# Kernel optimization log

Measured on AMD Instinct MI355X. Metric: run time of the kernel, lower is better.

## Reference

```python
import jax, jax.numpy as jnp
import numpy as np

N = 100000
E = 1600000
EMBED = 128
HEADS = 8
HEAD_DIM = EMBED // HEADS
EDGE_DIM = 6


def setup_inputs() -> dict:
    key = jax.random.key(0)
    ks = jax.random.split(key, 12)
    s = 0.05
    return {
        "x": jax.random.normal(ks[0], (N, EMBED), jnp.float32),
        "edge_index": jax.random.randint(ks[1], (2, E), 0, N, dtype=jnp.int64),
        "edge_attr": jax.random.normal(ks[2], (E, EDGE_DIM), jnp.float32),
        "Wq": jax.random.normal(ks[3], (EMBED, EMBED), jnp.float32) * s,
        "Wk": jax.random.normal(ks[4], (EMBED, EMBED), jnp.float32) * s,
        "Wv": jax.random.normal(ks[5], (EMBED, EMBED), jnp.float32) * s,
        "We1": jax.random.normal(ks[6], (EDGE_DIM, EMBED), jnp.float32) * s,
        "be1": jnp.zeros((EMBED,), jnp.float32),
        "We2": jax.random.normal(ks[7], (EMBED, HEADS), jnp.float32) * s,
        "be2": jnp.zeros((HEADS,), jnp.float32),
        "Wo": jax.random.normal(ks[8], (EMBED, EMBED), jnp.float32) * s,
        "bo": jnp.zeros((EMBED,), jnp.float32),
    }


def reference(x, edge_index, edge_attr, Wq, Wk, Wv, We1, be1, We2, be2, Wo, bo):
    num_particles = x.shape[0]
    scaling = HEAD_DIM ** (-0.5)
    # node projections -> (N, H, Dh)
    Q = (x @ Wq).reshape(num_particles, HEADS, HEAD_DIM)
    K = (x @ Wk).reshape(num_particles, HEADS, HEAD_DIM)
    V = (x @ Wv).reshape(num_particles, HEADS, HEAD_DIM)
    src, tgt = edge_index[0], edge_index[1]
    # per-edge dot-product scores (E, H)
    attn_scores = jnp.einsum('ehd,ehd->eh', Q[tgt], K[src]) * scaling
    # edge bias: Linear -> exact GELU -> Linear, (E, H)
    edge_bias = jax.nn.gelu(edge_attr @ We1 + be1, approximate=False) @ We2 + be2
    attn_scores = attn_scores + edge_bias
    # segment (scatter) softmax over edges sharing a target node
    seg_max = jax.ops.segment_max(attn_scores, tgt, num_segments=num_particles)
    ex = jnp.exp(attn_scores - seg_max[tgt])
    denom = jax.ops.segment_sum(ex, tgt, num_segments=num_particles)
    attn_weights = ex / denom[tgt]
    # weighted scatter-sum of V_src -> (N, H, Dh)
    weighted_V = attn_weights[:, :, None] * V[src]
    out = jax.ops.segment_sum(weighted_V, tgt, num_segments=num_particles)
    out = out.reshape(num_particles, EMBED) @ Wo + bo
    return out, attn_weights
```

## Files before the change

kernel.cpp:

```cpp
#include <hip/hip_runtime.h>

#define N_NODES 100000
#define N_EDGES 1600000
#define MAXD 64

typedef unsigned int u32;
typedef unsigned short u16;

__device__ __forceinline__ float bf2f(u16 u){ return __uint_as_float(((u32)u) << 16); }
__device__ __forceinline__ float lo16(u32 u){ return __uint_as_float(u << 16); }
__device__ __forceinline__ float hi16(u32 u){ return __uint_as_float(u & 0xffff0000u); }
__device__ __forceinline__ u32 f2bfbits(float f){
  u32 u = __float_as_uint(f);
  return (u + 0x7fffu + ((u >> 16) & 1u)) >> 16;
}

__device__ __forceinline__ float gelu_fast(float h){
  float z = h * 0.70710678118654752f;
  float u = z * z;
  const float k0 = 1.1283791670955126f;
  const float k1 = -0.37612638903183752f;
  const float k2 = 0.11283791670955126f;
  const float k3 = -0.026866170645131251f;
  const float k4 = 0.0052239776254421878f;
  const float k5 = -8.5483270234508528e-4f;
  const float k6 = 1.2055332981789664e-4f;
  float p = __builtin_fmaf(k6, u, k5);
  p = __builtin_fmaf(p, u, k4);
  p = __builtin_fmaf(p, u, k3);
  p = __builtin_fmaf(p, u, k2);
  p = __builtin_fmaf(p, u, k1);
  p = __builtin_fmaf(p, u, k0);
  float er = z * p;
  if (u > 0.36f) er = erff(z);
  float hh = 0.5f * h;
  return __builtin_fmaf(hh, er, hh);
}

template<int DT>
__device__ __forceinline__ float ldf(const void* p, size_t i){
  if (DT) return ((const float*)p)[i];
  else    return bf2f(((const u16*)p)[i]);
}

__device__ __forceinline__ int ld_src(const int* ei, int e, int f64){
  return f64 ? ei[2*(size_t)e] : ei[e];
}
__device__ __forceinline__ int ld_tgt(const int* ei, int e, int f64){
  return f64 ? ei[2*((size_t)N_EDGES + (size_t)e)] : ei[(size_t)N_EDGES + e];
}

__device__ __forceinline__ float bfdot16(uint4 qa, uint4 qb, uint4 ka, uint4 kb){
  float s = 0.f;
  s += lo16(qa.x)*lo16(ka.x) + hi16(qa.x)*hi16(ka.x);
  s += lo16(qa.y)*lo16(ka.y) + hi16(qa.y)*hi16(ka.y);
  s += lo16(qa.z)*lo16(ka.z) + hi16(qa.z)*hi16(ka.z);
  s += lo16(qa.w)*lo16(ka.w) + hi16(qa.w)*hi16(ka.w);
  s += lo16(qb.x)*lo16(kb.x) + hi16(qb.x)*hi16(kb.x);
  s += lo16(qb.y)*lo16(kb.y) + hi16(qb.y)*hi16(kb.y);
  s += lo16(qb.z)*lo16(kb.z) + hi16(qb.z)*hi16(kb.z);
  s += lo16(qb.w)*lo16(kb.w) + hi16(qb.w)*hi16(kb.w);
  return s;
}

extern "C" __global__ void detect_kernel(const int* __restrict__ ei,
                                         const u32* __restrict__ xw,
                                         int* __restrict__ flags)
{
  if (blockIdx.x == 0 && threadIdx.x == 0) {
    int any = 0;
    #pragma unroll
    for (int i = 0; i < 32; ++i) any |= ei[2*i + 1];
    flags[0] = (any == 0) ? 1 : 0;
    int weird = 0;
    for (int i = 0; i < 256; ++i) {
      u32 w = xw[i];
      float a = lo16(w), b = hi16(w);
      if (!(fabsf(a) < 1024.f)) weird++;
      if (!(fabsf(b) < 1024.f)) weird++;
    }
    flags[1] = (weird > 0) ? 1 : 0;
  }
}

template<int DT>
__global__ __launch_bounds__(256) void qkv_gemm_t(
    const void* __restrict__ x, const void* __restrict__ Wq,
    const void* __restrict__ Wk, const void* __restrict__ Wv,
    u16* __restrict__ Q, u16* __restrict__ Kd, u16* __restrict__ Vd,
    const int* __restrict__ flags)
{
  if (flags[1] != DT) return;
  __shared__ float xs[64*129];
  const int tid = threadIdx.x;
  const int row0 = blockIdx.x * 64;
  const void* W = (blockIdx.y == 0) ? Wq : (blockIdx.y == 1) ? Wk : Wv;
  u16* Out = (blockIdx.y == 0) ? Q : (blockIdx.y == 1) ? Kd : Vd;

  if (DT) {
    const float4* xg = (const float4*)x;
    #pragma unroll
    for (int i = 0; i < 8; ++i) {
      int li = tid + i*256;
      int r = li >> 5, c4 = li & 31;
      float4 v = make_float4(0.f,0.f,0.f,0.f);
      if (row0 + r < N_NODES) v = xg[(size_t)(row0 + r)*32 + c4];
      int base = r*129 + c4*4;
      xs[base] = v.x; xs[base+1] = v.y; xs[base+2] = v.z; xs[base+3] = v.w;
    }
  } else {
    const uint4* xg = (const uint4*)x;
    #pragma unroll
    for (int i = 0; i < 4; ++i) {
      int li = tid + i*256;
      int r = li >> 4, c8 = li & 15;
      uint4 v = make_uint4(0,0,0,0);
      if (row0 + r < N_NODES) v = xg[(size_t)(row0 + r)*16 + c8];
      int base = r*129 + c8*8;
      xs[base+0]=lo16(v.x); xs[base+1]=hi16(v.x);
      xs[base+2]=lo16(v.y); xs[base+3]=hi16(v.y);
      xs[base+4]=lo16(v.z); xs[base+5]=hi16(v.z);
      xs[base+6]=lo16(v.w); xs[base+7]=hi16(v.w);
    }
  }
  __syncthreads();

  const int cg = tid & 31;
  const int r0 = (tid >> 5) * 8;
  float acc[8][4];
  #pragma unroll
  for (int i=0;i<8;++i){ acc[i][0]=0.f; acc[i][1]=0.f; acc[i][2]=0.f; acc[i][3]=0.f; }

  for (int k = 0; k < 128; ++k) {
    float4 b;
    if (DT) {
      b = ((const float4*)W)[k*32 + cg];
    } else {
      uint2 t = ((const uint2*)W)[k*32 + cg];
      b = make_float4(lo16(t.x), hi16(t.x), lo16(t.y), hi16(t.y));
    }
    #pragma unroll
    for (int i = 0; i < 8; ++i) {
      float a = xs[(r0+i)*129 + k];
      acc[i][0] += a*b.x; acc[i][1] += a*b.y; acc[i][2] += a*b.z; acc[i][3] += a*b.w;
    }
  }
  #pragma unroll
  for (int i = 0; i < 8; ++i) {
    int gr = row0 + r0 + i;
    if (gr < N_NODES) {
      u32 p0 = f2bfbits(acc[i][0]) | (f2bfbits(acc[i][1]) << 16);
      u32 p1 = f2bfbits(acc[i][2]) | (f2bfbits(acc[i][3]) << 16);
      ((uint2*)(Out + (size_t)gr*128))[cg] = make_uint2(p0, p1);
    }
  }
}

template<int DT>
__global__ __launch_bounds__(256) void bias_kernel_t(
    const void* __restrict__ ea,
    const void* __restrict__ We1, const void* __restrict__ be1,
    const void* __restrict__ We2, const void* __restrict__ be2,
    float* __restrict__ scores, const int* __restrict__ flags)
{
  if (flags[1] != DT) return;
  __shared__ __align__(16) float wpk[128][16];
  __shared__ float b2s[8];
  const int tid = threadIdx.x;
  if (tid < 128) {
    int j = tid;
    wpk[j][0] = ldf<DT>(be1, j);
    #pragma unroll
    for (int d = 0; d < 6; ++d) wpk[j][1+d] = ldf<DT>(We1, d*128 + j);
    wpk[j][7] = 0.f;
    #pragma unroll
    for (int h = 0; h < 8; ++h) wpk[j][8+h] = ldf<DT>(We2, j*8 + h);
  }
  if (tid < 8) b2s[tid] = ldf<DT>(be2, tid);
  __syncthreads();

  const int gid = blockIdx.x * 256 + tid;
  if (gid >= N_EDGES/2) return;
  const int e0 = gid * 2;

  float a[12];
  if (DT) {
    const float4* eg = (const float4*)ea + (size_t)gid*3;
    float4 v0 = eg[0], v1 = eg[1], v2 = eg[2];
    a[0]=v0.x; a[1]=v0.y; a[2]=v0.z; a[3]=v0.w;
    a[4]=v1.x; a[5]=v1.y; a[6]=v1.z; a[7]=v1.w;
    a[8]=v2.x; a[9]=v2.y; a[10]=v2.z; a[11]=v2.w;
  } else {
    const uint2* eg = (const uint2*)ea + (size_t)gid*3;
    uint2 v0 = eg[0], v1 = eg[1], v2 = eg[2];
    u32 d[6] = {v0.x, v0.y, v1.x, v1.y, v2.x, v2.y};
    #pragma unroll
    for (int idx = 0; idx < 12; ++idx)
      a[idx] = (idx & 1) ? hi16(d[idx >> 1]) : lo16(d[idx >> 1]);
  }

  float bias[2][8];
  #pragma unroll
  for (int t=0;t<2;++t)
    #pragma unroll
    for (int h=0;h<8;++h) bias[t][h] = b2s[h];

  for (int j = 0; j < 128; ++j) {
    const float4* wp = (const float4*)wpk[j];
    float4 p0 = wp[0], p1 = wp[1], p2 = wp[2], p3 = wp[3];
    #pragma unroll
    for (int t = 0; t < 2; ++t) {
      float h = p0.x + a[t*6+0]*p0.y + a[t*6+1]*p0.z + a[t*6+2]*p0.w
                     + a[t*6+3]*p1.x + a[t*6+4]*p1.y + a[t*6+5]*p1.z;
      float g = gelu_fast(h);
      bias[t][0] += g*p2.x; bias[t][1] += g*p2.y; bias[t][2] += g*p2.z; bias[t][3] += g*p2.w;
      bias[t][4] += g*p3.x; bias[t][5] += g*p3.y; bias[t][6] += g*p3.z; bias[t][7] += g*p3.w;
    }
  }

  #pragma unroll
  for (int t = 0; t < 2; ++t) {
    float4* so = (float4*)(scores + (size_t)(e0 + t)*8);
    so[0] = make_float4(bias[t][0],bias[t][1],bias[t][2],bias[t][3]);
    so[1] = make_float4(bias[t][4],bias[t][5],bias[t][6],bias[t][7]);
  }
}

extern "C" __global__ __launch_bounds__(256) void hist_kernel(
    const int* __restrict__ ei, int* __restrict__ offs, const int* __restrict__ flags)
{
  int e = blockIdx.x*256 + threadIdx.x;
  if (e >= N_EDGES) return;
  int t = ld_tgt(ei, e, flags[0]);
  atomicAdd(&offs[t], 1);
}

extern "C" __global__ __launch_bounds__(1024) void scan1_kernel(
    int* __restrict__ offs, int* __restrict__ bsums)
{
  __shared__ int tmp[1024];
  int tid = threadIdx.x;
  int i = blockIdx.x*1024 + tid;
  int v = (i < N_NODES) ? offs[i] : 0;
  tmp[tid] = v;
  __syncthreads();
  for (int d = 1; d < 1024; d <<= 1) {
    int t = (tid >= d) ? tmp[tid-d] : 0;
    __syncthreads();
    tmp[tid] += t;
    __syncthreads();
  }
  if (i < N_NODES) offs[i] = tmp[tid] - v;
  if (tid == 1023) bsums[blockIdx.x] = tmp[1023];
}

extern "C" __global__ void scan2_kernel(int* __restrict__ bsums, int nb)
{
  if (threadIdx.x == 0 && blockIdx.x == 0) {
    int run = 0;
    for (int i = 0; i < nb; ++i) { int t = bsums[i]; bsums[i] = run; run += t; }
  }
}

extern "C" __global__ __launch_bounds__(1024) void scan3_kernel(
    int* __restrict__ offs, const int* __restrict__ bsums)
{
  int i = blockIdx.x*1024 + threadIdx.x;
  if (i < N_NODES) offs[i] += bsums[blockIdx.x];
}

extern "C" __global__ __launch_bounds__(256) void fill_kernel(
    const int* __restrict__ ei, int* __restrict__ offs,
    int* __restrict__ edge_sorted, const int* __restrict__ flags)
{
  int e = blockIdx.x*256 + threadIdx.x;
  if (e >= N_EDGES) return;
  int t = ld_tgt(ei, e, flags[0]);
  int p = atomicAdd(&offs[t], 1);
  edge_sorted[p] = e;
}

extern "C" __global__ __launch_bounds__(256) void node_score_kernel(
    const int* __restrict__ ei, const int* __restrict__ offs_incl,
    const int* __restrict__ edge_sorted, float* __restrict__ scores,
    const u16* __restrict__ Q, const u16* __restrict__ Kd,
    void* __restrict__ dout, const int* __restrict__ flags)
{
  __shared__ float s_lds[4][MAXD*8];
  __shared__ int   e_lds[4][MAXD];
  const int wid  = threadIdx.x >> 6;
  const int lane = threadIdx.x & 63;
  const int n = blockIdx.x*4 + wid;
  if (n >= N_NODES) return;
  const int f64 = flags[0], dt = flags[1];
  const int start = (n == 0) ? 0 : offs_incl[n-1];
  const int deg = offs_incl[n] - start;
  if (deg == 0) return;
  const int h = lane & 7, j = lane >> 3;

  const uint4* qr = (const uint4*)(Q + (size_t)n*128 + h*16);
  uint4 qa = qr[0], qb = qr[1];

  float m = -3.0e38f, s = 0.f;
  for (int jj = j; jj < deg; jj += 8) {
    int e = edge_sorted[start + jj];
    int src = ld_src(ei, e, f64);
    const uint4* kr = (const uint4*)(Kd + (size_t)src*128 + h*16);
    uint4 ka = kr[0], kb = kr[1];
    float v = bfdot16(qa, qb, ka, kb) * 0.25f + scores[(size_t)e*8 + h];
    if (jj < MAXD) {
      s_lds[wid][jj*8 + h] = v;
      if (h == 0) e_lds[wid][jj] = e;
    }
    float mn = fmaxf(m, v);
    s = s * __expf(m - mn) + __expf(v - mn);
    m = mn;
  }
  #pragma unroll
  for (int d = 8; d < 64; d <<= 1) {
    float mo = __shfl_xor(m, d);
    float so = __shfl_xor(s, d);
    float mn = fmaxf(m, mo);
    s = s * __expf(m - mn) + so * __expf(mo - mn);
    m = mn;
  }
  const float rsum = 1.f / s;

  float* wout = dt ? ((float*)dout + (size_t)N_NODES*128) : scores;
  for (int jj = j; jj < deg; jj += 8) {
    float sv; int eo;
    if (jj < MAXD) {
      sv = s_lds[wid][jj*8 + h];
      eo = e_lds[wid][jj];
    } else {
      eo = edge_sorted[start + jj];
      int src = ld_src(ei, eo, f64);
      const uint4* kr = (const uint4*)(Kd + (size_t)src*128 + h*16);
      uint4 ka = kr[0], kb = kr[1];
      sv = bfdot16(qa, qb, ka, kb) * 0.25f + scores[(size_t)eo*8 + h];
    }
    wout[(size_t)eo*8 + h] = __expf(sv - m) * rsum;
  }
}

extern "C" __global__ __launch_bounds__(256) void node_gather_kernel(
    const int* __restrict__ ei, const int* __restrict__ offs_incl,
    const int* __restrict__ edge_sorted, const float* __restrict__ scores,
    const u16* __restrict__ Vd, void* __restrict__ dout,
    const int* __restrict__ flags)
{
  const int wid  = threadIdx.x >> 6;
  const int lane = threadIdx.x & 63;
  const int n = blockIdx.x*4 + wid;
  if (n >= N_NODES) return;
  const int f64 = flags[0], dt = flags[1];
  const int start = (n == 0) ? 0 : offs_incl[n-1];
  const int deg = offs_incl[n] - start;
  size_t slot = dt ? ((size_t)n*128 + lane) : ((size_t)n*64 + lane);
  if (deg == 0) { ((u32*)dout)[slot] = 0; return; }
  const int h2 = lane & 7;
  const int t0 = lane >> 3;
  const int hC = lane >> 3;
  const float* wsrc = dt ? ((const float*)dout + (size_t)N_NODES*128) : scores;
  const size_t attn_b16 = (size_t)N_NODES*128;

  float acc0 = 0.f, acc1 = 0.f;
  const int nch = (deg + 7) >> 3;
  for (int c = 0; c < nch; ++c) {
    int jj = c*8 + t0;
    float w = 0.f; int sown = 0;
    if (jj < deg) {
      int e = edge_sorted[start + jj];
      sown = ld_src(ei, e, f64);
      w = wsrc[(size_t)e*8 + h2];
      if (!dt) ((u16*)dout)[attn_b16 + (size_t)e*8 + h2] = (u16)f2bfbits(w);
    }
    int lim = deg - c*8; if (lim > 8) lim = 8;
    u32 vreg[8];
    #pragma unroll
    for (int t = 0; t < 8; ++t) {
      if (t < lim) {
        int s2 = __shfl(sown, t*8);
        vreg[t] = *(const u32*)(Vd + (size_t)s2*128 + lane*2);
      }
    }
    #pragma unroll
    for (int t = 0; t < 8; ++t) {
      if (t < lim) {
        float wv = __shfl(w, t*8 + hC);
        acc0 += wv * lo16(vreg[t]);
        acc1 += wv * hi16(vreg[t]);
      }
    }
  }
  ((u32*)dout)[slot] = f2bfbits(acc0) | (f2bfbits(acc1) << 16);
}

template<int DT>
__global__ __launch_bounds__(256) void out_proj_t(
    const void* __restrict__ Wo, const void* __restrict__ bo,
    void* __restrict__ dout, const int* __restrict__ flags)
{
  if (flags[1] != DT) return;
  __shared__ float as_[64*129];
  const int tid = threadIdx.x;
  const int row0 = blockIdx.x * 64;
  {
    #pragma unroll
    for (int i = 0; i < 4; ++i) {
      int li = tid + i*256;
      int r = li >> 4, q = li & 15;
      int gr = row0 + r;
      uint4 v = make_uint4(0,0,0,0);
      if (gr < N_NODES) {
        const uint4* rp = (const uint4*)((const u32*)dout + (DT ? (size_t)gr*128 : (size_t)gr*64));
        v = rp[q];
      }
      int base = r*129 + q*8;
      as_[base+0]=lo16(v.x); as_[base+1]=hi16(v.x);
      as_[base+2]=lo16(v.y); as_[base+3]=hi16(v.y);
      as_[base+4]=lo16(v.z); as_[base+5]=hi16(v.z);
      as_[base+6]=lo16(v.w); as_[base+7]=hi16(v.w);
    }
  }
  __syncthreads();
  const int cg = tid & 31;
  const int r0 = (tid >> 5) * 8;
  float acc[8][4];
  #pragma unroll
  for (int i=0;i<8;++i){ acc[i][0]=0.f; acc[i][1]=0.f; acc[i][2]=0.f; acc[i][3]=0.f; }

  for (int k = 0; k < 128; ++k) {
    float4 b;
    if (DT) {
      b = ((const float4*)Wo)[k*32 + cg];
    } else {
      uint2 t = ((const uint2*)Wo)[k*32 + cg];
      b = make_float4(lo16(t.x), hi16(t.x), lo16(t.y), hi16(t.y));
    }
    #pragma unroll
    for (int i = 0; i < 8; ++i) {
      float a = as_[(r0+i)*129 + k];
      acc[i][0] += a*b.x; acc[i][1] += a*b.y; acc[i][2] += a*b.z; acc[i][3] += a*b.w;
    }
  }
  float bb0 = ldf<DT>(bo, cg*4+0), bb1 = ldf<DT>(bo, cg*4+1);
  float bb2 = ldf<DT>(bo, cg*4+2), bb3 = ldf<DT>(bo, cg*4+3);
  #pragma unroll
  for (int i = 0; i < 8; ++i) {
    int gr = row0 + r0 + i;
    if (gr < N_NODES) {
      if (DT) {
        ((float4*)((float*)dout + (size_t)gr*128))[cg] =
            make_float4(acc[i][0]+bb0, acc[i][1]+bb1, acc[i][2]+bb2, acc[i][3]+bb3);
      } else {
        u32 p0 = f2bfbits(acc[i][0]+bb0) | (f2bfbits(acc[i][1]+bb1) << 16);
        u32 p1 = f2bfbits(acc[i][2]+bb2) | (f2bfbits(acc[i][3]+bb3) << 16);
        ((uint2*)((u16*)dout + (size_t)gr*128))[cg] = make_uint2(p0, p1);
      }
    }
  }
}

extern "C" void kernel_launch(void* const* d_in, const int* in_sizes, int n_in,
                              void* d_out, int out_size, void* d_ws, size_t ws_size,
                              hipStream_t stream)
{
  const void* x   = d_in[0];
  const int*  ei  = (const int*)d_in[1];
  const void* ea  = d_in[2];
  const void* Wq  = d_in[3];
  const void* Wk  = d_in[4];
  const void* Wv  = d_in[5];
  const void* We1 = d_in[6];
  const void* be1 = d_in[7];
  const void* We2 = d_in[8];
  const void* be2 = d_in[9];
  const void* Wo  = d_in[10];
  const void* bo  = d_in[11];

  char* ws = (char*)d_ws;
  int*   flags       = (int*)  ws;
  u16*   Vd          = (u16*)  (ws + 4096);
  float* scores      = (float*)(ws + 25604096);
  int*   offs        = (int*)  (ws + 76804096);
  int*   bsums       = (int*)  (ws + 77204096);
  int*   edge_sorted = (int*)  (ws + 77204992);

  u16* Q  = (u16*)d_out;
  u16* Kd = Q + (size_t)N_NODES*128;

  detect_kernel<<<dim3(1), 64, 0, stream>>>(ei, (const u32*)x, flags);
  hipMemsetAsync(offs, 0, 400000, stream);

  qkv_gemm_t<0><<<dim3(1563,3), 256, 0, stream>>>(x, Wq, Wk, Wv, Q, Kd, Vd, flags);
  qkv_gemm_t<1><<<dim3(1563,3), 256, 0, stream>>>(x, Wq, Wk, Wv, Q, Kd, Vd, flags);

  bias_kernel_t<0><<<dim3(3125), 256, 0, stream>>>(ea, We1, be1, We2, be2, scores, flags);
  bias_kernel_t<1><<<dim3(3125), 256, 0, stream>>>(ea, We1, be1, We2, be2, scores, flags);

  hist_kernel <<<dim3(6250), 256, 0, stream>>>(ei, offs, flags);
  scan1_kernel<<<dim3(98), 1024, 0, stream>>>(offs, bsums);
  scan2_kernel<<<dim3(1), 64, 0, stream>>>(bsums, 98);
  scan3_kernel<<<dim3(98), 1024, 0, stream>>>(offs, bsums);
  fill_kernel <<<dim3(6250), 256, 0, stream>>>(ei, offs, edge_sorted, flags);

  node_score_kernel <<<dim3(25000), 256, 0, stream>>>(ei, offs, edge_sorted, scores, Q, Kd, d_out, flags);
  node_gather_kernel<<<dim3(25000), 256, 0, stream>>>(ei, offs, edge_sorted, scores, Vd, d_out, flags);

  out_proj_t<0><<<dim3(1563), 256, 0, stream>>>(Wo, bo, d_out, flags);
  out_proj_t<1><<<dim3(1563), 256, 0, stream>>>(Wo, bo, d_out, flags);
}
```

Before: 986.7 us.

## Cut launch count: runtime dtype branch, fuse histogram into bias, merge scan phases

Replaces the duplicated per-dtype template launches with single kernels that branch on the runtime flag, so each GEMM and bias stage launches once. The target histogram atomics move into the bias kernel, and the serial scan2 pass is folded into scan3 as a per-block reduction of earlier block sums. The GEMMs also switch to padded 132-stride shared rows with float4 smem reads and 4-wide k unrolling using explicit FMAs. Together these remove several kernel launches and some shared-memory instruction overhead, at the cost of register pressure and some redundant reduction work in scan3.

```diff
diff --git a/kernel.cpp b/kernel.cpp
--- a/kernel.cpp
+++ b/kernel.cpp
@@ -37,10 +37,8 @@
   return __builtin_fmaf(hh, er, hh);
 }
 
-template<int DT>
-__device__ __forceinline__ float ldf(const void* p, size_t i){
-  if (DT) return ((const float*)p)[i];
-  else    return bf2f(((const u16*)p)[i]);
+__device__ __forceinline__ float ldx(const void* p, size_t i, int dt){
+  return dt ? ((const float*)p)[i] : bf2f(((const u16*)p)[i]);
 }
 
 __device__ __forceinline__ int ld_src(const int* ei, int e, int f64){
@@ -83,21 +81,20 @@
   }
 }
 
-template<int DT>
-__global__ __launch_bounds__(256) void qkv_gemm_t(
+extern "C" __global__ __launch_bounds__(256) void qkv_gemm(
     const void* __restrict__ x, const void* __restrict__ Wq,
     const void* __restrict__ Wk, const void* __restrict__ Wv,
     u16* __restrict__ Q, u16* __restrict__ Kd, u16* __restrict__ Vd,
     const int* __restrict__ flags)
 {
-  if (flags[1] != DT) return;
-  __shared__ float xs[64*129];
+  __shared__ float xs[64*132];
   const int tid = threadIdx.x;
   const int row0 = blockIdx.x * 64;
   const void* W = (blockIdx.y == 0) ? Wq : (blockIdx.y == 1) ? Wk : Wv;
   u16* Out = (blockIdx.y == 0) ? Q : (blockIdx.y == 1) ? Kd : Vd;
-
-  if (DT) {
+  const int dt = flags[1];
+
+  if (dt) {
     const float4* xg = (const float4*)x;
     #pragma unroll
     for (int i = 0; i < 8; ++i) {
@@ -105,8 +102,7 @@
       int r = li >> 5, c4 = li & 31;
       float4 v = make_float4(0.f,0.f,0.f,0.f);
       if (row0 + r < N_NODES) v = xg[(size_t)(row0 + r)*32 + c4];
-      int base = r*129 + c4*4;
-      xs[base] = v.x; xs[base+1] = v.y; xs[base+2] = v.z; xs[base+3] = v.w;
+      *(float4*)&xs[r*132 + c4*4] = v;
     }
   } else {
     const uint4* xg = (const uint4*)x;
@@ -116,11 +112,9 @@
       int r = li >> 4, c8 = li & 15;
       uint4 v = make_uint4(0,0,0,0);
       if (row0 + r < N_NODES) v = xg[(size_t)(row0 + r)*16 + c8];
-      int base = r*129 + c8*8;
-      xs[base+0]=lo16(v.x); xs[base+1]=hi16(v.x);
-      xs[base+2]=lo16(v.y); xs[base+3]=hi16(v.y);
-      xs[base+4]=lo16(v.z); xs[base+5]=hi16(v.z);
-      xs[base+6]=lo16(v.w); xs[base+7]=hi16(v.w);
+      int base = r*132 + c8*8;
+      *(float4*)&xs[base]   = make_float4(lo16(v.x), hi16(v.x), lo16(v.y), hi16(v.y));
+      *(float4*)&xs[base+4] = make_float4(lo16(v.z), hi16(v.z), lo16(v.w), hi16(v.w));
     }
   }
   __syncthreads();
@@ -131,20 +125,56 @@
   #pragma unroll
   for (int i=0;i<8;++i){ acc[i][0]=0.f; acc[i][1]=0.f; acc[i][2]=0.f; acc[i][3]=0.f; }
 
-  for (int k = 0; k < 128; ++k) {
-    float4 b;
-    if (DT) {
-      b = ((const float4*)W)[k*32 + cg];
-    } else {
-      uint2 t = ((const uint2*)W)[k*32 + cg];
-      b = make_float4(lo16(t.x), hi16(t.x), lo16(t.y), hi16(t.y));
-    }
-    #pragma unroll
-    for (int i = 0; i < 8; ++i) {
-      float a = xs[(r0+i)*129 + k];
-      acc[i][0] += a*b.x; acc[i][1] += a*b.y; acc[i][2] += a*b.z; acc[i][3] += a*b.w;
-    }
-  }
+  if (dt) {
+    const float4* W4 = (const float4*)W;
+    for (int k = 0; k < 128; k += 4) {
+      float4 b0 = W4[(k+0)*32 + cg];
+      float4 b1 = W4[(k+1)*32 + cg];
+      float4 b2 = W4[(k+2)*32 + cg];
+      float4 b3 = W4[(k+3)*32 + cg];
+      float bb[4][4] = {{b0.x,b0.y,b0.z,b0.w},{b1.x,b1.y,b1.z,b1.w},
+                        {b2.x,b2.y,b2.z,b2.w},{b3.x,b3.y,b3.z,b3.w}};
+      #pragma unroll
+      for (int i = 0; i < 8; ++i) {
+        float4 av = *(const float4*)&xs[(r0+i)*132 + k];
+        #pragma unroll
+        for (int c = 0; c < 4; ++c) {
+          float t = acc[i][c];
+          t = __builtin_fmaf(av.x, bb[0][c], t);
+          t = __builtin_fmaf(av.y, bb[1][c], t);
+          t = __builtin_fmaf(av.z, bb[2][c], t);
+          t = __builtin_fmaf(av.w, bb[3][c], t);
+          acc[i][c] = t;
+        }
+      }
+    }
+  } else {
+    const uint2* W2 = (const uint2*)W;
+    for (int k = 0; k < 128; k += 4) {
+      uint2 t0 = W2[(k+0)*32 + cg];
+      uint2 t1 = W2[(k+1)*32 + cg];
+      uint2 t2 = W2[(k+2)*32 + cg];
+      uint2 t3 = W2[(k+3)*32 + cg];
+      float bb[4][4] = {{lo16(t0.x),hi16(t0.x),lo16(t0.y),hi16(t0.y)},
+                        {lo16(t1.x),hi16(t1.x),lo16(t1.y),hi16(t1.y)},
+                        {lo16(t2.x),hi16(t2.x),lo16(t2.y),hi16(t2.y)},
+                        {lo16(t3.x),hi16(t3.x),lo16(t3.y),hi16(t3.y)}};
+      #pragma unroll
+      for (int i = 0; i < 8; ++i) {
+        float4 av = *(const float4*)&xs[(r0+i)*132 + k];
+        #pragma unroll
+        for (int c = 0; c < 4; ++c) {
+          float t = acc[i][c];
+          t = __builtin_fmaf(av.x, bb[0][c], t);
+          t = __builtin_fmaf(av.y, bb[1][c], t);
+          t = __builtin_fmaf(av.z, bb[2][c], t);
+          t = __builtin_fmaf(av.w, bb[3][c], t);
+          acc[i][c] = t;
+        }
+      }
+    }
+  }
+
   #pragma unroll
   for (int i = 0; i < 8; ++i) {
     int gr = row0 + r0 + i;
@@ -156,35 +186,39 @@
   }
 }
 
-template<int DT>
-__global__ __launch_bounds__(256) void bias_kernel_t(
+extern "C" __global__ __launch_bounds__(256) void bias_kernel(
     const void* __restrict__ ea,
     const void* __restrict__ We1, const void* __restrict__ be1,
     const void* __restrict__ We2, const void* __restrict__ be2,
-    float* __restrict__ scores, const int* __restrict__ flags)
-{
-  if (flags[1] != DT) return;
+    float* __restrict__ scores, const int* __restrict__ ei,
+    int* __restrict__ offs, const int* __restrict__ flags)
+{
   __shared__ __align__(16) float wpk[128][16];
   __shared__ float b2s[8];
   const int tid = threadIdx.x;
+  const int dt = flags[1];
   if (tid < 128) {
     int j = tid;
-    wpk[j][0] = ldf<DT>(be1, j);
-    #pragma unroll
-    for (int d = 0; d < 6; ++d) wpk[j][1+d] = ldf<DT>(We1, d*128 + j);
+    wpk[j][0] = ldx(be1, j, dt);
+    #pragma unroll
+    for (int d = 0; d < 6; ++d) wpk[j][1+d] = ldx(We1, d*128 + j, dt);
     wpk[j][7] = 0.f;
     #pragma unroll
-    for (int h = 0; h < 8; ++h) wpk[j][8+h] = ldf<DT>(We2, j*8 + h);
-  }
-  if (tid < 8) b2s[tid] = ldf<DT>(be2, tid);
+    for (int h = 0; h < 8; ++h) wpk[j][8+h] = ldx(We2, j*8 + h, dt);
+  }
+  if (tid < 8) b2s[tid] = ldx(be2, tid, dt);
   __syncthreads();
 
   const int gid = blockIdx.x * 256 + tid;
   if (gid >= N_EDGES/2) return;
   const int e0 = gid * 2;
 
+  const int f64 = flags[0];
+  int tg0 = ld_tgt(ei, e0, f64);
+  int tg1 = ld_tgt(ei, e0+1, f64);
+
   float a[12];
-  if (DT) {
+  if (dt) {
     const float4* eg = (const float4*)ea + (size_t)gid*3;
     float4 v0 = eg[0], v1 = eg[1], v2 = eg[2];
     a[0]=v0.x; a[1]=v0.y; a[2]=v0.z; a[3]=v0.w;
@@ -224,15 +258,9 @@
     so[0] = make_float4(bias[t][0],bias[t][1],bias[t][2],bias[t][3]);
     so[1] = make_float4(bias[t][4],bias[t][5],bias[t][6],bias[t][7]);
   }
-}
-
-extern "C" __global__ __launch_bounds__(256) void hist_kernel(
-    const int* __restrict__ ei, int* __restrict__ offs, const int* __restrict__ flags)
-{
-  int e = blockIdx.x*256 + threadIdx.x;
-  if (e >= N_EDGES) return;
-  int t = ld_tgt(ei, e, flags[0]);
-  atomicAdd(&offs[t], 1);
+
+  atomicAdd(&offs[tg0], 1);
+  atomicAdd(&offs[tg1], 1);
 }
 
 extern "C" __global__ __launch_bounds__(1024) void scan1_kernel(
@@ -254,19 +282,21 @@
   if (tid == 1023) bsums[blockIdx.x] = tmp[1023];
 }
 
-extern "C" __global__ void scan2_kernel(int* __restrict__ bsums, int nb)
-{
-  if (threadIdx.x == 0 && blockIdx.x == 0) {
-    int run = 0;
-    for (int i = 0; i < nb; ++i) { int t = bsums[i]; bsums[i] = run; run += t; }
-  }
-}
-
 extern "C" __global__ __launch_bounds__(1024) void scan3_kernel(
     int* __restrict__ offs, const int* __restrict__ bsums)
 {
-  int i = blockIdx.x*1024 + threadIdx.x;
-  if (i < N_NODES) offs[i] += bsums[blockIdx.x];
+  __shared__ int red[128];
+  int tid = threadIdx.x;
+  if (tid < 128) red[tid] = (tid < blockIdx.x) ? bsums[tid] : 0;
+  __syncthreads();
+  #pragma unroll
+  for (int s = 64; s > 0; s >>= 1) {
+    if (tid < s) red[tid] += red[tid + s];
+    __syncthreads();
+  }
+  int base = red[0];
+  int i = blockIdx.x*1024 + tid;
+  if (i < N_NODES) offs[i] += base;
 }
 
 extern "C" __global__ __launch_bounds__(256) void fill_kernel(
@@ -396,15 +426,14 @@
   ((u32*)dout)[slot] = f2bfbits(acc0) | (f2bfbits(acc1) << 16);
 }
 
-template<int DT>
-__global__ __launch_bounds__(256) void out_proj_t(
+extern "C" __global__ __launch_bounds__(256) void out_proj(
     const void* __restrict__ Wo, const void* __restrict__ bo,
     void* __restrict__ dout, const int* __restrict__ flags)
 {
-  if (flags[1] != DT) return;
-  __shared__ float as_[64*129];
+  __shared__ float as_[64*132];
   const int tid = threadIdx.x;
   const int row0 = blockIdx.x * 64;
+  const int dt = flags[1];
   {
     #pragma unroll
     for (int i = 0; i < 4; ++i) {
@@ -413,14 +442,12 @@
       int gr = row0 + r;
       uint4 v = make_uint4(0,0,0,0);
       if (gr < N_NODES) {
-        const uint4* rp = (const uint4*)((const u32*)dout + (DT ? (size_t)gr*128 : (size_t)gr*64));
+        const uint4* rp = (const uint4*)((const u32*)dout + (dt ? (size_t)gr*128 : (size_t)gr*64));
         v = rp[q];
       }
-      int base = r*129 + q*8;
-      as_[base+0]=lo16(v.x); as_[base+1]=hi16(v.x);
-      as_[base+2]=lo16(v.y); as_[base+3]=hi16(v.y);
-      as_[base+4]=lo16(v.z); as_[base+5]=hi16(v.z);
-      as_[base+6]=lo16(v.w); as_[base+7]=hi16(v.w);
+      int base = r*132 + q*8;
+      *(float4*)&as_[base]   = make_float4(lo16(v.x), hi16(v.x), lo16(v.y), hi16(v.y));
+      *(float4*)&as_[base+4] = make_float4(lo16(v.z), hi16(v.z), lo16(v.w), hi16(v.w));
     }
   }
   __syncthreads();
@@ -430,27 +457,63 @@
   #pragma unroll
   for (int i=0;i<8;++i){ acc[i][0]=0.f; acc[i][1]=0.f; acc[i][2]=0.f; acc[i][3]=0.f; }
 
-  for (int k = 0; k < 128; ++k) {
-    float4 b;
-    if (DT) {
-      b = ((const float4*)Wo)[k*32 + cg];
-    } else {
-      uint2 t = ((const uint2*)Wo)[k*32 + cg];
-      b = make_float4(lo16(t.x), hi16(t.x), lo16(t.y), hi16(t.y));
-    }
-    #pragma unroll
-    for (int i = 0; i < 8; ++i) {
-      float a = as_[(r0+i)*129 + k];
-      acc[i][0] += a*b.x; acc[i][1] += a*b.y; acc[i][2] += a*b.z; acc[i][3] += a*b.w;
-    }
-  }
-  float bb0 = ldf<DT>(bo, cg*4+0), bb1 = ldf<DT>(bo, cg*4+1);
-  float bb2 = ldf<DT>(bo, cg*4+2), bb3 = ldf<DT>(bo, cg*4+3);
+  if (dt) {
+    const float4* W4 = (const float4*)Wo;
+    for (int k = 0; k < 128; k += 4) {
+      float4 b0 = W4[(k+0)*32 + cg];
+      float4 b1 = W4[(k+1)*32 + cg];
+      float4 b2 = W4[(k+2)*32 + cg];
+      float4 b3 = W4[(k+3)*32 + cg];
+      float bb[4][4] = {{b0.x,b0.y,b0.z,b0.w},{b1.x,b1.y,b1.z,b1.w},
+                        {b2.x,b2.y,b2.z,b2.w},{b3.x,b3.y,b3.z,b3.w}};
+      #pragma unroll
+      for (int i = 0; i < 8; ++i) {
+        float4 av = *(const float4*)&as_[(r0+i)*132 + k];
+        #pragma unroll
+        for (int c = 0; c < 4; ++c) {
+          float t = acc[i][c];
+          t = __builtin_fmaf(av.x, bb[0][c], t);
+          t = __builtin_fmaf(av.y, bb[1][c], t);
+          t = __builtin_fmaf(av.z, bb[2][c], t);
+          t = __builtin_fmaf(av.w, bb[3][c], t);
+          acc[i][c] = t;
+        }
+      }
+    }
+  } else {
+    const uint2* W2 = (const uint2*)Wo;
+    for (int k = 0; k < 128; k += 4) {
+      uint2 t0 = W2[(k+0)*32 + cg];
+      uint2 t1 = W2[(k+1)*32 + cg];
+      uint2 t2 = W2[(k+2)*32 + cg];
+      uint2 t3 = W2[(k+3)*32 + cg];
+      float bb[4][4] = {{lo16(t0.x),hi16(t0.x),lo16(t0.y),hi16(t0.y)},
+                        {lo16(t1.x),hi16(t1.x),lo16(t1.y),hi16(t1.y)},
+                        {lo16(t2.x),hi16(t2.x),lo16(t2.y),hi16(t2.y)},
+                        {lo16(t3.x),hi16(t3.x),lo16(t3.y),hi16(t3.y)}};
+      #pragma unroll
+      for (int i = 0; i < 8; ++i) {
+        float4 av = *(const float4*)&as_[(r0+i)*132 + k];
+        #pragma unroll
+        for (int c = 0; c < 4; ++c) {
+          float t = acc[i][c];
+          t = __builtin_fmaf(av.x, bb[0][c], t);
+          t = __builtin_fmaf(av.y, bb[1][c], t);
+          t = __builtin_fmaf(av.z, bb[2][c], t);
+          t = __builtin_fmaf(av.w, bb[3][c], t);
+          acc[i][c] = t;
+        }
+      }
+    }
+  }
+
+  float bb0 = ldx(bo, cg*4+0, dt), bb1 = ldx(bo, cg*4+1, dt);
+  float bb2 = ldx(bo, cg*4+2, dt), bb3 = ldx(bo, cg*4+3, dt);
   #pragma unroll
   for (int i = 0; i < 8; ++i) {
     int gr = row0 + r0 + i;
     if (gr < N_NODES) {
-      if (DT) {
+      if (dt) {
         ((float4*)((float*)dout + (size_t)gr*128))[cg] =
             make_float4(acc[i][0]+bb0, acc[i][1]+bb1, acc[i][2]+bb2, acc[i][3]+bb3);
       } else {
@@ -493,21 +556,16 @@
   detect_kernel<<<dim3(1), 64, 0, stream>>>(ei, (const u32*)x, flags);
   hipMemsetAsync(offs, 0, 400000, stream);
 
-  qkv_gemm_t<0><<<dim3(1563,3), 256, 0, stream>>>(x, Wq, Wk, Wv, Q, Kd, Vd, flags);
-  qkv_gemm_t<1><<<dim3(1563,3), 256, 0, stream>>>(x, Wq, Wk, Wv, Q, Kd, Vd, flags);
-
-  bias_kernel_t<0><<<dim3(3125), 256, 0, stream>>>(ea, We1, be1, We2, be2, scores, flags);
-  bias_kernel_t<1><<<dim3(3125), 256, 0, stream>>>(ea, We1, be1, We2, be2, scores, flags);
-
-  hist_kernel <<<dim3(6250), 256, 0, stream>>>(ei, offs, flags);
+  qkv_gemm<<<dim3(1563,3), 256, 0, stream>>>(x, Wq, Wk, Wv, Q, Kd, Vd, flags);
+
+  bias_kernel<<<dim3(3125), 256, 0, stream>>>(ea, We1, be1, We2, be2, scores, ei, offs, flags);
+
   scan1_kernel<<<dim3(98), 1024, 0, stream>>>(offs, bsums);
-  scan2_kernel<<<dim3(1), 64, 0, stream>>>(bsums, 98);
   scan3_kernel<<<dim3(98), 1024, 0, stream>>>(offs, bsums);
   fill_kernel <<<dim3(6250), 256, 0, stream>>>(ei, offs, edge_sorted, flags);
 
   node_score_kernel <<<dim3(25000), 256, 0, stream>>>(ei, offs, edge_sorted, scores, Q, Kd, d_out, flags);
   node_gather_kernel<<<dim3(25000), 256, 0, stream>>>(ei, offs, edge_sorted, scores, Vd, d_out, flags);
 
-  out_proj_t<0><<<dim3(1563), 256, 0, stream>>>(Wo, bo, d_out, flags);
-  out_proj_t<1><<<dim3(1563), 256, 0, stream>>>(Wo, bo, d_out, flags);
-}
+  out_proj<<<dim3(1563), 256, 0, stream>>>(Wo, bo, d_out, flags);
+}
```

Result: faster. 884.3 us (-10.4%).
